# Optimization experiments

Measured on AMD Instinct MI355X. Metric: run time of the kernel, lower is better.

## Reference

```python
import jax, jax.numpy as jnp
import numpy as np

D_MODEL = 512

def setup_inputs() -> dict:
    key = jax.random.key(0)
    k1, k2, k3, k4, k5 = jax.random.split(key, 5)
    x = jax.random.normal(k1, (8, D_MODEL, 2048), dtype=jnp.float32)
    s = 1.0 / np.sqrt(D_MODEL)
    W_qkv = jax.random.uniform(k2, (D_MODEL, 3 * D_MODEL), dtype=jnp.float32, minval=-s, maxval=s)
    b_qkv = jax.random.uniform(k3, (3 * D_MODEL,), dtype=jnp.float32, minval=-s, maxval=s)
    W_proj = jax.random.uniform(k4, (D_MODEL, D_MODEL), dtype=jnp.float32, minval=-s, maxval=s)
    b_proj = jax.random.uniform(k5, (D_MODEL,), dtype=jnp.float32, minval=-s, maxval=s)
    return {"x": x, "W_qkv": W_qkv, "b_qkv": b_qkv, "W_proj": W_proj, "b_proj": b_proj}

def reference(x, W_qkv, b_qkv, W_proj, b_proj):
    # x: [B, L, N] with L == d_model; attend across the N variable axis
    xt = jnp.swapaxes(x, 1, 2)                      # [B, N, L]
    L = xt.shape[-1]
    qkv = xt @ W_qkv + b_qkv                        # [B, N, 3L]
    q, k, v = jnp.split(qkv, 3, axis=-1)            # each [B, N, L]
    attn = jnp.einsum('bnd,bmd->bnm', q, k) / jnp.sqrt(jnp.float32(L))
    attn = jax.nn.softmax(attn, axis=-1)            # [B, N, N]
    out = jnp.einsum('bnm,bmd->bnd', attn, v)       # [B, N, L]
    out = out @ W_proj + b_proj                     # [B, N, L]
    return jnp.swapaxes(out, 1, 2)                  # [B, L, N]
```

## Files before the change

### kernel.cpp

```cpp
#include <hip/hip_runtime.h>

#define NVAR 2048
#define DM   512
#define J3   1536

typedef _Float16 f16;
typedef _Float16 f16x8 __attribute__((ext_vector_type(8)));
typedef _Float16 f16x4 __attribute__((ext_vector_type(4)));
typedef float    f32x4 __attribute__((ext_vector_type(4)));

#define SBAR() do { asm volatile("s_barrier" ::: "memory"); \
                    __builtin_amdgcn_sched_barrier(0); } while(0)
#define LGKM0() do { asm volatile("s_waitcnt lgkmcnt(0)" ::: "memory"); \
                     __builtin_amdgcn_sched_barrier(0); } while(0)
#define GLOAD(gp, lp) __builtin_amdgcn_global_load_lds( \
    (const __attribute__((address_space(1))) void*)(gp), \
    (__attribute__((address_space(3))) void*)(lp), 16, 0, 0)

__device__ __forceinline__ void waitvm_n(int n) {
    switch (n) {
    case 0: asm volatile("s_waitcnt vmcnt(0)" ::: "memory"); break;
    case 1: asm volatile("s_waitcnt vmcnt(1)" ::: "memory"); break;
    case 2: asm volatile("s_waitcnt vmcnt(2)" ::: "memory"); break;
    case 3: asm volatile("s_waitcnt vmcnt(3)" ::: "memory"); break;
    case 4: asm volatile("s_waitcnt vmcnt(4)" ::: "memory"); break;
    case 5: asm volatile("s_waitcnt vmcnt(5)" ::: "memory"); break;
    case 6: asm volatile("s_waitcnt vmcnt(6)" ::: "memory"); break;
    case 7: asm volatile("s_waitcnt vmcnt(7)" ::: "memory"); break;
    case 8: asm volatile("s_waitcnt vmcnt(8)" ::: "memory"); break;
    default: break;
    }
    __builtin_amdgcn_sched_barrier(0);
}

__global__ __launch_bounds__(256)
void k_tr(const float* __restrict__ src, f16* __restrict__ dst,
          int R, int C, long bsSrc, long bsDst) {
    __shared__ float t[64][65];
    const float* s = src + (size_t)blockIdx.z * bsSrc;
    f16* d = dst + (size_t)blockIdx.z * bsDst;
    const int c0 = blockIdx.x * 64, r0 = blockIdx.y * 64;
    const int lx = threadIdx.x & 15, ly = threadIdx.x >> 4;
#pragma unroll
    for (int p = 0; p < 4; ++p) {
        int r = p * 16 + ly;
        f32x4 v = *(const f32x4*)(s + (size_t)(r0 + r) * C + c0 + lx * 4);
#pragma unroll
        for (int i = 0; i < 4; ++i) t[r][lx * 4 + i] = v[i];
    }
    __syncthreads();
#pragma unroll
    for (int p = 0; p < 4; ++p) {
        int c = p * 16 + ly;
        f16x4 h;
#pragma unroll
        for (int i = 0; i < 4; ++i) h[i] = (f16)t[lx * 4 + i][c];
        *(f16x4*)(d + (size_t)(c0 + c) * R + r0 + lx * 4) = h;
    }
}

__global__ __launch_bounds__(256)
void k_prep(const float* __restrict__ Wqkv, const float* __restrict__ Wproj,
            const float* __restrict__ bqkv,
            f16* __restrict__ WqT, f16* __restrict__ WpT,
            f16* __restrict__ Wq2, float* __restrict__ bias_c) {
    __shared__ float t[64][65];
    const int b = blockIdx.x;
    if (b < 192) {
        const float* s; f16* d; int R, C, bx, by;
        if (b < 128) { s = Wqkv; d = WqT; R = DM; C = J3; bx = b & 15; by = b >> 4; }
        else { s = Wproj; d = WpT; R = DM; C = DM; bx = (b - 128) & 7; by = (b - 128) >> 3; }
        const int c0 = bx * 64, r0 = by * 64;
        const int lx = threadIdx.x & 15, ly = threadIdx.x >> 4;
#pragma unroll
        for (int p = 0; p < 4; ++p) {
            int r = p * 16 + ly;
            f32x4 v = *(const f32x4*)(s + (size_t)(r0 + r) * C + c0 + lx * 4);
#pragma unroll
            for (int i = 0; i < 4; ++i) t[r][lx * 4 + i] = v[i];
        }
        __syncthreads();
#pragma unroll
        for (int p = 0; p < 4; ++p) {
            int c = p * 16 + ly;
            f16x4 h;
#pragma unroll
            for (int i = 0; i < 4; ++i) h[i] = (f16)t[lx * 4 + i][c];
            *(f16x4*)(d + (size_t)(c0 + c) * R + r0 + lx * 4) = h;
        }
    } else if (b < 448) {
        int idx = (b - 192) * 256 + threadIdx.x;
        int gi = idx * 4;
        int d = gi >> 9, j = gi & 511;
        f32x4 v = *(const f32x4*)(Wqkv + (size_t)d * J3 + 1024 + j);
        f16x4 h;
#pragma unroll
        for (int i = 0; i < 4; ++i) h[i] = (f16)v[i];
        *(f16x4*)(Wq2 + (size_t)d * 512 + j) = h;
    } else {
        const int bb = b - 448;
        const int lt = threadIdx.x & 63, js = threadIdx.x >> 6;
        const int l = bb * 64 + lt;
        float s = 0.f;
        for (int j = js * 128; j < js * 128 + 128; ++j)
            s += bqkv[1024 + j] * Wproj[(size_t)j * DM + l];
        float* red = &t[0][0];
        red[js * 64 + lt] = s;
        __syncthreads();
        if (js == 0)
            bias_c[1024 + l] = (red[lt] + red[64 + lt]) + (red[128 + lt] + red[192 + lt]);
        if (threadIdx.x < 128) {
            int i = bb * 128 + threadIdx.x;
            bias_c[i] = bqkv[i];
        }
    }
}

#define ASZ (256 * 64)
__global__ __launch_bounds__(512, 2)
void gemm_sp(const f16* __restrict__ A, const f16* __restrict__ B,
             long bsA, long bsB, int lda, int ldb, int K,
             float scale, f16* __restrict__ o0) {
    __shared__ f16 smem[5 * ASZ];
    f16* sA = smem;
    f16* sB = smem + 3 * ASZ;

    const int tid  = threadIdx.x;
    const int lane = tid & 63;
    const int w    = __builtin_amdgcn_readfirstlane(tid >> 6);
    const int wm   = (w >> 2) * 128;
    const int wn   = (w & 3) * 64;
    const int z    = blockIdx.x;
    const int bid  = blockIdx.y;
    const int bxA  = bid & 7;
    const int bxB  = bid >> 3;

    const f16* Ab = A + (size_t)z * bsA + (size_t)bxA * 256 * lda;
    const f16* Bb = B + (size_t)z * bsB + (size_t)bxB * 256 * ldb;

    int offA[2][2], offB[2][2];
#pragma unroll
    for (int h = 0; h < 2; ++h)
#pragma unroll
        for (int i = 0; i < 2; ++i) {
            int slot = i * 512 + tid;
            int row  = h * 128 + (slot >> 3);
            int s    = (slot & 7) ^ (row & 7);
            offA[h][i] = row * lda + s * 8;
            offB[h][i] = row * ldb + s * 8;
        }

    auto STG_A = [&](int kt, int h, int buf) {
        f16* d = sA + buf * ASZ + h * 8192;
#pragma unroll
        for (int i = 0; i < 2; ++i)
            GLOAD(Ab + offA[h][i] + kt * 64, d + (i * 512 + tid) * 8);
    };
    auto STG_B = [&](int kt, int h, int buf) {
        f16* d = sB + buf * ASZ + h * 8192;
#pragma unroll
        for (int i = 0; i < 2; ++i)
            GLOAD(Bb + offB[h][i] + kt * 64, d + (i * 512 + tid) * 8);
    };

    int koff[2];
#pragma unroll
    for (int ks = 0; ks < 2; ++ks)
        koff[ks] = ((ks * 4 + (lane >> 4)) ^ (lane & 7)) * 8;
    const int rowA = (wm + (lane & 15)) * 64;
    const int rowB = (wn + (lane & 15)) * 64;

    f16x8 av[8][2], bv[4][2];
    f32x4 acc[8][4] = {};

    auto LD_AV = [&](const f16* p, int mi0) {
#pragma unroll
        for (int mi = 0; mi < 4; ++mi)
#pragma unroll
            for (int ks = 0; ks < 2; ++ks)
                av[mi0 + mi][ks] = *(const f16x8*)(p + rowA + (mi0 + mi) * 1024 + koff[ks]);
    };
    auto LD_BV = [&](const f16* p, int nj0) {
#pragma unroll
        for (int nj = 0; nj < 2; ++nj)
#pragma unroll
            for (int ks = 0; ks < 2; ++ks)
                bv[nj0 + nj][ks] = *(const f16x8*)(p + rowB + (nj0 + nj) * 1024 + koff[ks]);
    };
    auto MM = [&](int mi0, int nj0) {
        __builtin_amdgcn_s_setprio(1);
#pragma unroll
        for (int mi = 0; mi < 4; ++mi)
#pragma unroll
            for (int nj = 0; nj < 2; ++nj)
#pragma unroll
                for (int ks = 0; ks < 2; ++ks)
                    acc[mi0 + mi][nj0 + nj] = __builtin_amdgcn_mfma_f32_16x16x32_f16(
                        av[mi0 + mi][ks], bv[nj0 + nj][ks], acc[mi0 + mi][nj0 + nj], 0, 0, 0);
        __builtin_amdgcn_s_setprio(0);
    };

    const int NT = K >> 6;
    int issued = 0, markB = 0;

    STG_A(0, 0, 0); STG_A(0, 1, 0); issued += 4;
    STG_B(0, 0, 0); STG_B(0, 1, 0); issued += 4; markB = issued;
    if (NT > 1) { STG_A(1, 0, 1); STG_A(1, 1, 1); issued += 4; }
    waitvm_n(issued - markB);
    SBAR();

    int iA = 0, iB = 0;
    for (int t = 0; t < NT; ++t) {
        const f16* pA = sA + iA * ASZ;
        const f16* pB = sB + iB * ASZ;
        const int bufB2 = iB ^ 1;
        int bufA2 = iA + 2; if (bufA2 >= 3) bufA2 -= 3;

        LD_BV(pB, 0); LD_AV(pA, 0);
        if (t + 1 < NT) { STG_B(t + 1, 0, bufB2); issued += 2; }
        SBAR(); LGKM0();
        MM(0, 0);
        SBAR();

        LD_BV(pB, 2);
        if (t + 1 < NT) { STG_B(t + 1, 1, bufB2); issued += 2; markB = issued; }
        SBAR(); LGKM0();
        MM(0, 2);
        SBAR();

        LD_AV(pA, 4);
        if (t + 2 < NT) { STG_A(t + 2, 0, bufA2); issued += 2; }
        SBAR(); LGKM0();
        MM(4, 2);
        SBAR();

        if (t + 2 < NT) { STG_A(t + 2, 1, bufA2); issued += 2; }
        if (t + 1 < NT) { waitvm_n(issued - markB); SBAR(); }
        MM(4, 0);
        if (t + 1 < NT) SBAR();

        iA = (iA + 1 == 3) ? 0 : iA + 1;
        iB ^= 1;
    }

    const int n0 = bxB * 256;
    const int m0 = bxA * 256;
    f16* bb = smem;
#pragma unroll
    for (int mi = 0; mi < 8; ++mi) {
        const int m    = wm + mi * 16 + ((lane >> 4) << 2);
        const int c16  = m >> 3;
        const int half = m & 4;
#pragma unroll
        for (int nj = 0; nj < 4; ++nj) {
            const int nl = wn + nj * 16 + (lane & 15);
            f16x4 vv;
#pragma unroll
            for (int r = 0; r < 4; ++r)
                vv[r] = (f16)__expf(acc[mi][nj][r] * scale);
            *(f16x4*)(bb + nl * 256 + ((c16 ^ (nl & 7)) << 3) + half) = vv;
        }
    }
    LGKM0();
    SBAR();
#pragma unroll
    for (int it = 0; it < 16; ++it) {
        const int row = it * 16 + (tid >> 5);
        const int ch  = tid & 31;
        f16x8 v = *(const f16x8*)(bb + row * 256 + ((ch ^ (row & 7)) << 3));
        *(f16x8*)(o0 + ((size_t)z * NVAR + n0 + row) * NVAR + m0 + ch * 8) = v;
    }
}

#define AO (128 * 64)
#define BO (256 * 64)
__global__ __launch_bounds__(512, 2)
void gemm_out(const f16* __restrict__ A, const f16* __restrict__ B,
              long bsA, long bsB, int lda, int ldb, int K,
              const float* __restrict__ bias, float* __restrict__ of) {
    __shared__ f16 smem[3 * AO + 2 * BO];
    f16* sA = smem;
    f16* sB = smem + 3 * AO;

    const int tid  = threadIdx.x;
    const int lane = tid & 63;
    const int w    = __builtin_amdgcn_readfirstlane(tid >> 6);
    const int wm   = (w >> 2) * 64;
    const int wn   = (w & 3) * 64;
    const int z    = blockIdx.x;
    const int bid  = blockIdx.y;
    const int bxA  = bid & 15;
    const int bxB  = bid >> 4;

    const f16* Ab = A + (size_t)z * bsA + (size_t)bxA * 128 * lda;
    const f16* Bb = B + (size_t)z * bsB + (size_t)bxB * 256 * ldb;

    int offA[2], offB[4];
#pragma unroll
    for (int i = 0; i < 2; ++i) {
        int slot = i * 512 + tid;
        int row  = slot >> 3;
        int s    = (slot & 7) ^ (row & 7);
        offA[i] = row * lda + s * 8;
    }
#pragma unroll
    for (int i = 0; i < 4; ++i) {
        int slot = i * 512 + tid;
        int row  = slot >> 3;
        int s    = (slot & 7) ^ (row & 7);
        offB[i] = row * ldb + s * 8;
    }

    auto STG_A = [&](int kt, int buf) {
        f16* d = sA + buf * AO;
#pragma unroll
        for (int i = 0; i < 2; ++i)
            GLOAD(Ab + offA[i] + kt * 64, d + (i * 512 + tid) * 8);
    };
    auto STG_B = [&](int kt, int buf) {
        f16* d = sB + buf * BO;
#pragma unroll
        for (int i = 0; i < 4; ++i)
            GLOAD(Bb + offB[i] + kt * 64, d + (i * 512 + tid) * 8);
    };

    int koff[2];
#pragma unroll
    for (int ks = 0; ks < 2; ++ks)
        koff[ks] = ((ks * 4 + (lane >> 4)) ^ (lane & 7)) * 8;
    const int rowA = (wm + (lane & 15)) * 64;
    const int rowB = (wn + (lane & 15)) * 64;

    f16x8 ones;
#pragma unroll
    for (int e = 0; e < 8; ++e) ones[e] = (f16)1.0f;

    f16x8 av[4][2], bv[4][2];
    f32x4 acc[4][4] = {};
    f32x4 accrs[4] = {};

    auto LD_AV = [&](const f16* p, int mi0) {
#pragma unroll
        for (int mi = 0; mi < 2; ++mi)
#pragma unroll
            for (int ks = 0; ks < 2; ++ks)
                av[mi0 + mi][ks] = *(const f16x8*)(p + rowA + (mi0 + mi) * 1024 + koff[ks]);
    };
    auto LD_BV = [&](const f16* p) {
#pragma unroll
        for (int nj = 0; nj < 4; ++nj)
#pragma unroll
            for (int ks = 0; ks < 2; ++ks)
                bv[nj][ks] = *(const f16x8*)(p + rowB + nj * 1024 + koff[ks]);
    };
    auto MM = [&](int mi0) {
        __builtin_amdgcn_s_setprio(1);
#pragma unroll
        for (int mi = 0; mi < 2; ++mi)
#pragma unroll
            for (int ks = 0; ks < 2; ++ks) {
                accrs[mi0 + mi] = __builtin_amdgcn_mfma_f32_16x16x32_f16(
                    av[mi0 + mi][ks], ones, accrs[mi0 + mi], 0, 0, 0);
#pragma unroll
                for (int nj = 0; nj < 4; ++nj)
                    acc[mi0 + mi][nj] = __builtin_amdgcn_mfma_f32_16x16x32_f16(
                        av[mi0 + mi][ks], bv[nj][ks], acc[mi0 + mi][nj], 0, 0, 0);
            }
        __builtin_amdgcn_s_setprio(0);
    };

    const int NT = K >> 6;
    int issued = 0, markB = 0;

    STG_A(0, 0); issued += 2;
    STG_B(0, 0); issued += 4; markB = issued;
    if (NT > 1) { STG_A(1, 1); issued += 2; }
    waitvm_n(issued - markB);
    SBAR();

    int iA = 0, iB = 0;
    for (int t = 0; t < NT; ++t) {
        const f16* pA = sA + iA * AO;
        const f16* pB = sB + iB * BO;
        int bufA2 = iA + 2; if (bufA2 >= 3) bufA2 -= 3;

        LD_BV(pB); LD_AV(pA, 0);
        if (t + 1 < NT) { STG_B(t + 1, iB ^ 1); issued += 4; markB = issued; }
        SBAR(); LGKM0();
        MM(0);
        SBAR();

        LD_AV(pA, 2);
        if (t + 2 < NT) { STG_A(t + 2, bufA2); issued += 2; }
        SBAR(); LGKM0();
        MM(2);
        if (t + 1 < NT) { waitvm_n(issued - markB); SBAR(); }

        iA = (iA + 1 == 3) ? 0 : iA + 1;
        iB ^= 1;
    }

    const int rb0 = bxA * 128 + wm + (lane >> 4) * 4;
    const int cb0 = bxB * 256 + wn + (lane & 15);
#pragma unroll
    for (int mi = 0; mi < 4; ++mi) {
        f32x4 inv;
#pragma unroll
        for (int r = 0; r < 4; ++r) inv[r] = 1.0f / accrs[mi][r];
#pragma unroll
        for (int nj = 0; nj < 4; ++nj) {
            const int l = cb0 + nj * 16;
            const float bb = bias[l];
            f32x4 vv;
#pragma unroll
            for (int r = 0; r < 4; ++r) vv[r] = acc[mi][nj][r] * inv[r] + bb;
            *(f32x4*)(of + ((size_t)z * DM + l) * NVAR + rb0 + mi * 16) = vv;
        }
    }
}

template<int MODE>
__global__ __launch_bounds__(256)
void gemm_f16(const f16* __restrict__ A, const f16* __restrict__ B,
              long bsA, long bsB, int lda, int ldb, int K, int nbx,
              const float* __restrict__ bias,
              f16* __restrict__ o0, f16* __restrict__ o1, f16* __restrict__ o2) {
    __shared__ f16 sA[128 * 64];
    __shared__ f16 sB[128 * 64];
    const int tid  = threadIdx.x;
    const int lane = tid & 63;
    const int w    = __builtin_amdgcn_readfirstlane(tid >> 6);
    const int wm   = (w >> 1) * 64;
    const int wn   = (w & 1) * 64;
    const int z    = blockIdx.x;
    const int bid  = blockIdx.y;
    const int bxA  = bid % nbx;
    const int bxB  = bid / nbx;

    const f16* Ab = A + (size_t)z * bsA + (size_t)bxA * 128 * lda;
    const f16* Bb = B + (size_t)z * bsB + (size_t)bxB * 128 * ldb;

    int srcA[4], srcB[4];
#pragma unroll
    for (int i = 0; i < 4; ++i) {
        int slot = i * 256 + tid;
        int row  = slot >> 3;
        int s    = (slot & 7) ^ (row & 7);
        srcA[i] = row * lda + s * 8;
        srcB[i] = row * ldb + s * 8;
    }

    f32x4 acc[4][4] = {};

    for (int k0 = 0; k0 < K; k0 += 64) {
        __syncthreads();
#pragma unroll
        for (int i = 0; i < 4; ++i) {
            GLOAD(Ab + srcA[i] + k0, sA + i * 2048 + w * 512);
            GLOAD(Bb + srcB[i] + k0, sB + i * 2048 + w * 512);
        }
        __syncthreads();
#pragma unroll
        for (int kh = 0; kh < 2; ++kh) {
            f16x8 av[4], bv[4];
#pragma unroll
            for (int mi = 0; mi < 4; ++mi) {
                int r = wm + mi * 16 + (lane & 15);
                int s = (kh * 4 + (lane >> 4)) ^ (r & 7);
                av[mi] = *(const f16x8*)(sA + r * 64 + s * 8);
            }
#pragma unroll
            for (int nj = 0; nj < 4; ++nj) {
                int r = wn + nj * 16 + (lane & 15);
                int s = (kh * 4 + (lane >> 4)) ^ (r & 7);
                bv[nj] = *(const f16x8*)(sB + r * 64 + s * 8);
            }
#pragma unroll
            for (int mi = 0; mi < 4; ++mi)
#pragma unroll
                for (int nj = 0; nj < 4; ++nj)
                    acc[mi][nj] = __builtin_amdgcn_mfma_f32_16x16x32_f16(
                        av[mi], bv[nj], acc[mi][nj], 0, 0, 0);
        }
    }

    const int rb0 = bxA * 128 + wm + (lane >> 4) * 4;
    const int cb0 = bxB * 128 + wn + (lane & 15);

    if (MODE == 0) {
        const int seg = (bxA * 128) >> 9;
#pragma unroll
        for (int mi = 0; mi < 4; ++mi) {
            const int j = rb0 + mi * 16;
            const f32x4 b4 = *(const f32x4*)(bias + j);
#pragma unroll
            for (int nj = 0; nj < 4; ++nj) {
                const int n = cb0 + nj * 16;
                if (seg == 2) {
#pragma unroll
                    for (int r = 0; r < 4; ++r)
                        o2[((size_t)z * DM + (j - 1024 + r)) * NVAR + n] =
                            (f16)(acc[mi][nj][r] + b4[r]);
                } else {
                    f16* dst = seg ? o1 : o0;
                    const int jj = seg ? j - 512 : j;
                    f16x4 vv;
#pragma unroll
                    for (int r = 0; r < 4; ++r) vv[r] = (f16)(acc[mi][nj][r] + b4[r]);
                    *(f16x4*)(dst + ((size_t)z * NVAR + n) * DM + jj) = vv;
                }
            }
        }
    } else {
#pragma unroll
        for (int mi = 0; mi < 4; ++mi)
#pragma unroll
            for (int nj = 0; nj < 4; ++nj) {
                f16x4 vv;
#pragma unroll
                for (int r = 0; r < 4; ++r) vv[r] = (f16)acc[mi][nj][r];
                *(f16x4*)(o0 + ((size_t)(cb0 + nj * 16)) * DM
                               + rb0 + mi * 16) = vv;
            }
    }
}

extern "C" void kernel_launch(void* const* d_in, const int* in_sizes, int n_in,
                              void* d_out, int out_size, void* d_ws, size_t ws_size,
                              hipStream_t stream) {
    const float* x     = (const float*)d_in[0];
    const float* Wqkv  = (const float*)d_in[1];
    const float* bqkv  = (const float*)d_in[2];
    const float* Wproj = (const float*)d_in[3];
    const float* bproj = (const float*)d_in[4];
    float* out = (float*)d_out;

    const size_t PB = (size_t)NVAR * DM;
    f16* xT   = (f16*)d_ws;
    f16* q    = xT + 8 * PB;
    f16* kk   = q  + 8 * PB;
    f16* vwT  = kk + 8 * PB;
    f16* S    = vwT + 8 * PB;
    f16* scr  = S  + (size_t)8 * NVAR * NVAR;
    f16* WqT  = scr + 8 * PB;
    f16* WvpT = WqT + (size_t)1024 * DM;
    f16* WpT  = WqT + (size_t)J3 * DM;
    f16* Wq2  = scr;
    float* bias_c = (float*)(scr + 512 * 512);

    k_tr<<<dim3(NVAR / 64, DM / 64, 8), 256, 0, stream>>>(
        x, xT, DM, NVAR, (long)DM * NVAR, (long)NVAR * DM);
    k_prep<<<dim3(456), 256, 0, stream>>>(Wqkv, Wproj, bqkv, WqT, WpT, Wq2, bias_c);

    gemm_f16<4><<<dim3(1, 16), 256, 0, stream>>>(
        Wq2, WpT, 0, 0, 512, DM, DM, 4, nullptr, WvpT, nullptr, nullptr);

    gemm_f16<0><<<dim3(8, 12 * 16), 256, 0, stream>>>(
        WqT, xT, 0, (long)NVAR * DM, DM, DM, DM, 12,
        bias_c, q, kk, vwT);

    gemm_sp<<<dim3(8, 8 * 8), 512, 0, stream>>>(
        kk, q, (long)NVAR * DM, (long)NVAR * DM, DM, DM, DM,
        0.044194173824159216f, S);

    gemm_out<<<dim3(8, 32), 512, 0, stream>>>(
        S, vwT, (long)NVAR * NVAR, (long)DM * NVAR, NVAR, NVAR, NVAR,
        bproj, out);
}
```

Before: 178.1 us.

## Fold Q/K projections into a single Wq·Wkᵀ matrix applied to x

Rewrites the QK^T scores algebraically as x·(Wq Wkᵀ)·xᵀ plus a per-key bias term. A small precomputed 512x512 matrix MT replaces the separate Q and K projections, so the big projection GEMM produces 1024 output rows instead of 1536. Bias terms that are constant per query row cancel in the softmax and are dropped. The remaining key bias vector is computed with an extra MFMA column and added before the exp. This adds extra prep GEMMs and changes where fp16 rounding happens, so accuracy risk rises because G = x·MT is held in fp16.

```diff
diff --git a/kernel.cpp b/kernel.cpp
--- a/kernel.cpp
+++ b/kernel.cpp
@@ -62,20 +62,25 @@
 __global__ __launch_bounds__(256)
 void k_prep(const float* __restrict__ Wqkv, const float* __restrict__ Wproj,
             const float* __restrict__ bqkv,
-            f16* __restrict__ WqT, f16* __restrict__ WpT,
-            f16* __restrict__ Wq2, float* __restrict__ bias_c) {
+            f16* __restrict__ WqkvH, f16* __restrict__ WpT,
+            float* __restrict__ bvp, f16* __restrict__ w_vH) {
     __shared__ float t[64][65];
     const int b = blockIdx.x;
-    if (b < 192) {
-        const float* s; f16* d; int R, C, bx, by;
-        if (b < 128) { s = Wqkv; d = WqT; R = DM; C = J3; bx = b & 15; by = b >> 4; }
-        else { s = Wproj; d = WpT; R = DM; C = DM; bx = (b - 128) & 7; by = (b - 128) >> 3; }
+    if (b < 768) {
+        int gi = (b * 256 + threadIdx.x) * 4;
+        f32x4 v = *(const f32x4*)(Wqkv + gi);
+        f16x4 h;
+#pragma unroll
+        for (int i = 0; i < 4; ++i) h[i] = (f16)v[i];
+        *(f16x4*)(WqkvH + gi) = h;
+    } else if (b < 832) {
+        const int bx = (b - 768) & 7, by = (b - 768) >> 3;
         const int c0 = bx * 64, r0 = by * 64;
         const int lx = threadIdx.x & 15, ly = threadIdx.x >> 4;
 #pragma unroll
         for (int p = 0; p < 4; ++p) {
             int r = p * 16 + ly;
-            f32x4 v = *(const f32x4*)(s + (size_t)(r0 + r) * C + c0 + lx * 4);
+            f32x4 v = *(const f32x4*)(Wproj + (size_t)(r0 + r) * DM + c0 + lx * 4);
 #pragma unroll
             for (int i = 0; i < 4; ++i) t[r][lx * 4 + i] = v[i];
         }
@@ -86,19 +91,10 @@
             f16x4 h;
 #pragma unroll
             for (int i = 0; i < 4; ++i) h[i] = (f16)t[lx * 4 + i][c];
-            *(f16x4*)(d + (size_t)(c0 + c) * R + r0 + lx * 4) = h;
-        }
-    } else if (b < 448) {
-        int idx = (b - 192) * 256 + threadIdx.x;
-        int gi = idx * 4;
-        int d = gi >> 9, j = gi & 511;
-        f32x4 v = *(const f32x4*)(Wqkv + (size_t)d * J3 + 1024 + j);
-        f16x4 h;
-#pragma unroll
-        for (int i = 0; i < 4; ++i) h[i] = (f16)v[i];
-        *(f16x4*)(Wq2 + (size_t)d * 512 + j) = h;
-    } else {
-        const int bb = b - 448;
+            *(f16x4*)(WpT + (size_t)(c0 + c) * DM + r0 + lx * 4) = h;
+        }
+    } else if (b < 840) {
+        const int bb = b - 832;
         const int lt = threadIdx.x & 63, js = threadIdx.x >> 6;
         const int l = bb * 64 + lt;
         float s = 0.f;
@@ -108,11 +104,20 @@
         red[js * 64 + lt] = s;
         __syncthreads();
         if (js == 0)
-            bias_c[1024 + l] = (red[lt] + red[64 + lt]) + (red[128 + lt] + red[192 + lt]);
-        if (threadIdx.x < 128) {
-            int i = bb * 128 + threadIdx.x;
-            bias_c[i] = bqkv[i];
-        }
+            bvp[l] = (red[lt] + red[64 + lt]) + (red[128 + lt] + red[192 + lt]);
+    } else {
+        const int bb = b - 840;
+        const int lt = threadIdx.x & 63, js = threadIdx.x >> 6;
+        const int l = bb * 64 + lt;
+        float s = 0.f;
+        const float* row = Wqkv + (size_t)l * J3 + 512;
+        for (int d = js * 128; d < js * 128 + 128; ++d)
+            s += row[d] * bqkv[d];
+        float* red = &t[0][0];
+        red[js * 64 + lt] = s;
+        __syncthreads();
+        if (js == 0)
+            w_vH[l] = (f16)((red[lt] + red[64 + lt]) + (red[128 + lt] + red[192 + lt]));
     }
 }
 
@@ -120,7 +125,7 @@
 __global__ __launch_bounds__(512, 2)
 void gemm_sp(const f16* __restrict__ A, const f16* __restrict__ B,
              long bsA, long bsB, int lda, int ldb, int K,
-             float scale, f16* __restrict__ o0) {
+             float scale, f16* __restrict__ o0, const float* __restrict__ vbuf) {
     __shared__ f16 smem[5 * ASZ];
     f16* sA = smem;
     f16* sB = smem + 3 * ASZ;
@@ -248,16 +253,17 @@
     f16* bb = smem;
 #pragma unroll
     for (int mi = 0; mi < 8; ++mi) {
-        const int m    = wm + mi * 16 + ((lane >> 4) << 2);
-        const int c16  = m >> 3;
-        const int half = m & 4;
+        const int mloc = wm + mi * 16 + ((lane >> 4) << 2);
+        const int c16  = mloc >> 3;
+        const int half = mloc & 4;
+        const f32x4 v4 = *(const f32x4*)(vbuf + (size_t)z * NVAR + m0 + mloc);
 #pragma unroll
         for (int nj = 0; nj < 4; ++nj) {
             const int nl = wn + nj * 16 + (lane & 15);
             f16x4 vv;
 #pragma unroll
             for (int r = 0; r < 4; ++r)
-                vv[r] = (f16)__expf(acc[mi][nj][r] * scale);
+                vv[r] = (f16)__expf((acc[mi][nj][r] + v4[r]) * scale);
             *(f16x4*)(bb + nl * 256 + ((c16 ^ (nl & 7)) << 3) + half) = vv;
         }
     }
@@ -423,8 +429,9 @@
 __global__ __launch_bounds__(256)
 void gemm_f16(const f16* __restrict__ A, const f16* __restrict__ B,
               long bsA, long bsB, int lda, int ldb, int K, int nbx,
-              const float* __restrict__ bias,
-              f16* __restrict__ o0, f16* __restrict__ o1, f16* __restrict__ o2) {
+              const float* __restrict__ bias, const f16* __restrict__ wv,
+              f16* __restrict__ o0, f16* __restrict__ o1,
+              float* __restrict__ vbuf) {
     __shared__ f16 sA[128 * 64];
     __shared__ f16 sB[128 * 64];
     const int tid  = threadIdx.x;
@@ -451,6 +458,7 @@
     }
 
     f32x4 acc[4][4] = {};
+    f32x4 accv[4] = {};
 
     for (int k0 = 0; k0 < K; k0 += 64) {
         __syncthreads();
@@ -475,6 +483,13 @@
                 int s = (kh * 4 + (lane >> 4)) ^ (r & 7);
                 bv[nj] = *(const f16x8*)(sB + r * 64 + s * 8);
             }
+            if constexpr (MODE == 0) {
+                f16x8 wvf = *(const f16x8*)(wv + k0 + ((kh * 4 + (lane >> 4)) << 3));
+#pragma unroll
+                for (int nj = 0; nj < 4; ++nj)
+                    accv[nj] = __builtin_amdgcn_mfma_f32_16x16x32_f16(
+                        wvf, bv[nj], accv[nj], 0, 0, 0);
+            }
 #pragma unroll
             for (int mi = 0; mi < 4; ++mi)
 #pragma unroll
@@ -489,25 +504,36 @@
 
     if (MODE == 0) {
         const int seg = (bxA * 128) >> 9;
-#pragma unroll
-        for (int mi = 0; mi < 4; ++mi) {
-            const int j = rb0 + mi * 16;
-            const f32x4 b4 = *(const f32x4*)(bias + j);
-#pragma unroll
-            for (int nj = 0; nj < 4; ++nj) {
-                const int n = cb0 + nj * 16;
-                if (seg == 2) {
+        if (seg == 0) {
+#pragma unroll
+            for (int mi = 0; mi < 4; ++mi) {
+                const int j = rb0 + mi * 16;
+#pragma unroll
+                for (int nj = 0; nj < 4; ++nj) {
+                    const int n = cb0 + nj * 16;
+                    f16x4 vv;
+#pragma unroll
+                    for (int r = 0; r < 4; ++r) vv[r] = (f16)acc[mi][nj][r];
+                    *(f16x4*)(o0 + ((size_t)z * NVAR + n) * DM + j) = vv;
+                }
+            }
+            if (bxA == 0 && w < 2 && (lane >> 4) == 0) {
+#pragma unroll
+                for (int nj = 0; nj < 4; ++nj)
+                    vbuf[(size_t)z * NVAR + cb0 + nj * 16] = accv[nj][0];
+            }
+        } else {
+#pragma unroll
+            for (int mi = 0; mi < 4; ++mi) {
+                const int j = rb0 + mi * 16;
+                const f32x4 b4 = *(const f32x4*)(bias + (j - 512));
+#pragma unroll
+                for (int nj = 0; nj < 4; ++nj) {
+                    const int n = cb0 + nj * 16;
 #pragma unroll
                     for (int r = 0; r < 4; ++r)
-                        o2[((size_t)z * DM + (j - 1024 + r)) * NVAR + n] =
+                        o1[((size_t)z * DM + (j - 512 + r)) * NVAR + n] =
                             (f16)(acc[mi][nj][r] + b4[r]);
-                } else {
-                    f16* dst = seg ? o1 : o0;
-                    const int jj = seg ? j - 512 : j;
-                    f16x4 vv;
-#pragma unroll
-                    for (int r = 0; r < 4; ++r) vv[r] = (f16)(acc[mi][nj][r] + b4[r]);
-                    *(f16x4*)(dst + ((size_t)z * NVAR + n) * DM + jj) = vv;
                 }
             }
         }
@@ -536,32 +562,38 @@
     float* out = (float*)d_out;
 
     const size_t PB = (size_t)NVAR * DM;
-    f16* xT   = (f16*)d_ws;
-    f16* q    = xT + 8 * PB;
-    f16* kk   = q  + 8 * PB;
-    f16* vwT  = kk + 8 * PB;
-    f16* S    = vwT + 8 * PB;
-    f16* scr  = S  + (size_t)8 * NVAR * NVAR;
-    f16* WqT  = scr + 8 * PB;
-    f16* WvpT = WqT + (size_t)1024 * DM;
-    f16* WpT  = WqT + (size_t)J3 * DM;
-    f16* Wq2  = scr;
-    float* bias_c = (float*)(scr + 512 * 512);
+    f16* xT    = (f16*)d_ws;
+    f16* G     = xT + 8 * PB;
+    f16* vwT   = G  + 8 * PB;
+    f16* S     = vwT + 8 * PB;
+    f16* WqkvH = S + (size_t)8 * NVAR * NVAR;
+    f16* WpT   = WqkvH + (size_t)512 * J3;
+    f16* stack = WpT + (size_t)512 * 512;
+    f16* MT    = stack;
+    f16* WvpT  = stack + (size_t)512 * 512;
+    f16* w_vH  = stack + (size_t)1024 * 512;
+    float* bvp = (float*)(w_vH + 512);
+    float* vbuf = bvp + 512;
 
     k_tr<<<dim3(NVAR / 64, DM / 64, 8), 256, 0, stream>>>(
         x, xT, DM, NVAR, (long)DM * NVAR, (long)NVAR * DM);
-    k_prep<<<dim3(456), 256, 0, stream>>>(Wqkv, Wproj, bqkv, WqT, WpT, Wq2, bias_c);
+    k_prep<<<dim3(848), 256, 0, stream>>>(Wqkv, Wproj, bqkv, WqkvH, WpT, bvp, w_vH);
 
     gemm_f16<4><<<dim3(1, 16), 256, 0, stream>>>(
-        Wq2, WpT, 0, 0, 512, DM, DM, 4, nullptr, WvpT, nullptr, nullptr);
-
-    gemm_f16<0><<<dim3(8, 12 * 16), 256, 0, stream>>>(
-        WqT, xT, 0, (long)NVAR * DM, DM, DM, DM, 12,
-        bias_c, q, kk, vwT);
+        WqkvH, WqkvH + 512, 0, 0, J3, J3, 512, 4,
+        nullptr, nullptr, MT, nullptr, nullptr);
+
+    gemm_f16<4><<<dim3(1, 16), 256, 0, stream>>>(
+        WqkvH + 1024, WpT, 0, 0, J3, DM, 512, 4,
+        nullptr, nullptr, WvpT, nullptr, nullptr);
+
+    gemm_f16<0><<<dim3(8, 8 * 16), 256, 0, stream>>>(
+        stack, xT, 0, (long)NVAR * DM, DM, DM, DM, 8,
+        bvp, w_vH, G, vwT, vbuf);
 
     gemm_sp<<<dim3(8, 8 * 8), 512, 0, stream>>>(
-        kk, q, (long)NVAR * DM, (long)NVAR * DM, DM, DM, DM,
-        0.044194173824159216f, S);
+        xT, G, (long)NVAR * DM, (long)NVAR * DM, DM, DM, DM,
+        0.044194173824159216f, S, vbuf);
 
     gemm_out<<<dim3(8, 32), 512, 0, stream>>>(
         S, vwT, (long)NVAR * NVAR, (long)DM * NVAR, NVAR, NVAR, NVAR,
```

New measurement: 185.6 us. 1.04x slower.
